# Performance work log

Measured on AMD Instinct MI355X. Metric: run time of the kernel, lower is better.

## Reference

```python
import jax, jax.numpy as jnp
import numpy as np

NUM_EXPERTS = 64
TOP_K = 2


def setup_inputs() -> dict:
    key = jax.random.key(0)
    k1, k2 = jax.random.split(key)
    B, D, E = 16384, 4096, NUM_EXPERTS
    routing_features = jax.random.normal(k1, (B, D), dtype=jnp.float32)
    # nn.Linear(D, E, bias=False) weight: [E, D], kaiming-uniform-ish init
    bound = 1.0 / np.sqrt(D)
    gate_w = jax.random.uniform(k2, (E, D), dtype=jnp.float32, minval=-bound, maxval=bound)
    return {"routing_features": routing_features, "gate_w": gate_w}


def reference(routing_features, gate_w):
    B = routing_features.shape[0]
    E, K = NUM_EXPERTS, TOP_K
    # linear gate (no bias): [B, E]
    logits = jnp.einsum("bd,ed->be", routing_features, gate_w)
    full_probs = jax.nn.softmax(logits, axis=-1)
    top_k_logits, top_k_indices = jax.lax.top_k(logits, K)  # [B, K]
    top_k_weights = jax.nn.softmax(top_k_logits, axis=-1)
    # load-balance loss: f_i = fraction of (token, slot) assignments to expert i
    tokens_per_expert = jnp.zeros((E,), dtype=jnp.float32).at[top_k_indices.reshape(-1)].add(1.0)
    f = tokens_per_expert / (B * K)
    P = full_probs.mean(axis=0)
    aux_loss = E * jnp.sum(f * P)
    return top_k_weights, top_k_indices, aux_loss
```

## Files before the change

kernel.cpp:

```cpp
#include <hip/hip_runtime.h>
#include <math.h>


typedef __attribute__((ext_vector_type(8))) short bf16x8;
typedef __attribute__((ext_vector_type(4))) float f32x4;

constexpr int B_ROWS  = 16384;
constexpr int D_DIM   = 4096;
constexpr int E_EXP   = 64;
constexpr int NTHR    = 512;
constexpr int TM      = 128;
constexpr int KSEG    = 256;
constexpr int NSPLIT  = D_DIM / KSEG;
constexpr int NS      = KSEG / 32;
constexpr int FLAGCAP = 8192;
constexpr float GAPTHR = 1e-3f;

__device__ __forceinline__ float wave_max64(float v) {
#pragma unroll
  for (int m = 32; m >= 1; m >>= 1) v = fmaxf(v, __shfl_xor(v, m, 64));
  return v;
}
__device__ __forceinline__ float wave_sum64(float v) {
#pragma unroll
  for (int m = 32; m >= 1; m >>= 1) v += __shfl_xor(v, m, 64);
  return v;
}
__device__ __forceinline__ void wave_argmax64(float v, int i, float& mv, int& mi) {
#pragma unroll
  for (int m = 32; m >= 1; m >>= 1) {
    float ov = __shfl_xor(v, m, 64);
    int   oi = __shfl_xor(i, m, 64);
    if (ov > v || (ov == v && oi < i)) { v = ov; i = oi; }
  }
  mv = v; mi = i;
}

__device__ __forceinline__ void async_copy16(void* lds_dst, const void* g_src) {
  auto g = (const __attribute__((address_space(1))) char*)(g_src);
  auto l = (__attribute__((address_space(3))) char*)(lds_dst);
  __builtin_amdgcn_global_load_lds(g, l, 16, 0, 0);
}

__device__ __forceinline__ void split8(const f32x4 a, const f32x4 b, bf16x8& hi, bf16x8& lo) {
  float f[8] = {a[0], a[1], a[2], a[3], b[0], b[1], b[2], b[3]};
#pragma unroll
  for (int i = 0; i < 8; ++i) {
    unsigned int u = __float_as_uint(f[i]);
    hi[i] = (short)(u >> 16);
    float rem = f[i] - __uint_as_float(u & 0xffff0000u);
    lo[i] = (short)(__float_as_uint(rem) >> 16);
  }
}

__global__ __launch_bounds__(NTHR) void wsplit(const float* __restrict__ gw,
                                               char* __restrict__ wsW,
                                               unsigned int* __restrict__ hdr) {
  const int n = blockIdx.x;
  const int t = threadIdx.x;
  if (n == 0 && t < 192) hdr[t] = 0u;
  const int lane = t & 63, h = (t >> 6) & 1, wc = t >> 7;
  const int col = wc * 16 + (lane & 15);
  const int k0  = n * 32 + (lane >> 4) * 8;
  const float* src = gw + (size_t)col * D_DIM + k0;
  union { unsigned short us[8]; uint4 v; } pk;
#pragma unroll
  for (int i = 0; i < 8; ++i) {
    float f = src[i];
    unsigned int u = __float_as_uint(f);
    if (h == 0) {
      pk.us[i] = (unsigned short)(u >> 16);
    } else {
      float rem = f - __uint_as_float(u & 0xffff0000u);
      pk.us[i] = (unsigned short)(__float_as_uint(rem) >> 16);
    }
  }
  *(uint4*)(wsW + (size_t)n * 8192 + (size_t)t * 16) = pk.v;
}

__global__ __launch_bounds__(NTHR) void gemm_partial(
    const float* __restrict__ rf, const char* __restrict__ wsW,
    float* __restrict__ part) {
  __shared__ char wlds[NS * 8192] __attribute__((aligned(16)));

  const int t = threadIdx.x, lane = t & 63, wv = t >> 6;
  const int ks   = blockIdx.x >> 7;
  const int rb   = blockIdx.x & 127;
  const int row0 = rb * TM;

  {
    const char* src = wsW + (size_t)ks * (NS * 8192);
#pragma unroll
    for (int i = 0; i < NS; ++i)
      async_copy16(wlds + i * 8192 + t * 16, src + i * 8192 + t * 16);
  }
  __syncthreads();

  const float* aptr = rf + (size_t)(row0 + wv * 16 + (lane & 15)) * D_DIM
                         + ks * KSEG + (lane >> 4) * 8;

  f32x4 acc[4] = {{0.f,0.f,0.f,0.f},{0.f,0.f,0.f,0.f},{0.f,0.f,0.f,0.f},{0.f,0.f,0.f,0.f}};
  f32x4 a0[4], a1[4];

#define LDA(s, n) { a0[s] = *(const f32x4*)(aptr + (n) * 32); \
                    a1[s] = *(const f32x4*)(aptr + (n) * 32 + 4); }

  LDA(0, 0); LDA(1, 1); LDA(2, 2); LDA(3, 3);
  __builtin_amdgcn_sched_barrier(0);

#pragma unroll
  for (int n = 0; n < NS; ++n) {
    const int s = n & 3;
    bf16x8 ahi, alo;
    split8(a0[s], a1[s], ahi, alo);
    if (n + 4 < NS) LDA(s, n + 4);
    __builtin_amdgcn_sched_barrier(0);
    const char* wn = wlds + n * 8192 + lane * 16;
#pragma unroll
    for (int cb = 0; cb < 4; ++cb) {
      bf16x8 whi = *(const bf16x8*)(wn + cb * 2048);
      bf16x8 wlo = *(const bf16x8*)(wn + cb * 2048 + 1024);
      acc[cb] = __builtin_amdgcn_mfma_f32_16x16x32_bf16(ahi, whi, acc[cb], 0, 0, 0);
      acc[cb] = __builtin_amdgcn_mfma_f32_16x16x32_bf16(alo, whi, acc[cb], 0, 0, 0);
      acc[cb] = __builtin_amdgcn_mfma_f32_16x16x32_bf16(ahi, wlo, acc[cb], 0, 0, 0);
    }
    __builtin_amdgcn_sched_barrier(0);
  }
#undef LDA

  const int colb = lane & 15;
  const int rowb = (lane >> 4) * 4;
  float* dst = part + ((size_t)ks * B_ROWS + row0 + wv * 16 + rowb) * E_EXP + colb;
#pragma unroll
  for (int cb = 0; cb < 4; ++cb)
#pragma unroll
    for (int j = 0; j < 4; ++j)
      dst[(size_t)j * E_EXP + cb * 16] = acc[cb][j];
}

__global__ __launch_bounds__(NTHR) void epilogue(
    const float* __restrict__ part, float* __restrict__ out,
    float* __restrict__ psum, unsigned int* __restrict__ cnt,
    int* __restrict__ flagcnt, int* __restrict__ flaglist) {
  __shared__ float pcol[E_EXP];
  __shared__ unsigned int scnt[E_EXP];

  const int t = threadIdx.x, lane = t & 63, wv = t >> 6;
  const int row0 = blockIdx.x * 64;

  if (t < E_EXP) { scnt[t] = 0; pcol[t] = 0.f; }
  __syncthreads();

#pragma unroll
  for (int j = 0; j < 8; ++j) {
    const int row = row0 + wv * 8 + j;
    float lg = 0.f;
#pragma unroll
    for (int s = 0; s < NSPLIT; ++s)
      lg += part[((size_t)s * B_ROWS + row) * E_EXP + lane];

    const float m  = wave_max64(lg);
    const float p  = __expf(lg - m);
    const float ss = wave_sum64(p);
    atomicAdd(&pcol[lane], p / ss);

    float v1; int i1; wave_argmax64(lg, lane, v1, i1);
    const float lm1 = (lane == i1) ? -INFINITY : lg;
    float v2; int i2; wave_argmax64(lm1, lane, v2, i2);
    const float lm2 = (lane == i2) ? -INFINITY : lm1;
    float v3; int i3; wave_argmax64(lm2, lane, v3, i3);
    if (lane == 0) {
      const float ex = expf(v2 - v1);
      out[row * 2 + 0] = 1.f / (1.f + ex);
      out[row * 2 + 1] = ex / (1.f + ex);
      out[2 * B_ROWS + row * 2 + 0] = (float)i1;
      out[2 * B_ROWS + row * 2 + 1] = (float)i2;
      atomicAdd(&scnt[i1], 1u);
      atomicAdd(&scnt[i2], 1u);
      if (v1 - v2 < GAPTHR || v2 - v3 < GAPTHR) {
        int fi = atomicAdd(flagcnt, 1);
        if (fi < FLAGCAP) flaglist[fi] = row;
      }
    }
  }
  __syncthreads();
  if (t < E_EXP) {
    atomicAdd(&psum[t], pcol[t]);
    const unsigned int c = scnt[t];
    if (c) atomicAdd(&cnt[t], c);
  }
}

__global__ __launch_bounds__(256) void cleanup(
    const float* __restrict__ rf, const float* __restrict__ gw,
    const int* __restrict__ flagcnt, const int* __restrict__ flaglist,
    const float* __restrict__ psum, const unsigned int* __restrict__ cnt,
    float* __restrict__ out) {
  __shared__ double sm[256];
  const int t = threadIdx.x;
  if (blockIdx.x == 0 && t < 64) {
    const float f = (float)cnt[t] / (float)(B_ROWS * 2);
    const float P = psum[t] / (float)B_ROWS;
    float v = wave_sum64(f * P);
    if (t == 0) out[4 * B_ROWS] = (float)E_EXP * v;
  }
  const int nf = min(*flagcnt, FLAGCAP);
  for (int fi = blockIdx.x; fi < nf; fi += gridDim.x) {
    const int row = flaglist[fi];
    const int e = t & 63, seg = t >> 6;
    const float* a = rf + (size_t)row * D_DIM + seg * 1024;
    const float* w = gw + (size_t)e * D_DIM + seg * 1024;
    double p0 = 0.0, p1 = 0.0, p2 = 0.0, p3 = 0.0;
    for (int k = 0; k < 1024; k += 4) {
      p0 = fma((double)a[k + 0], (double)w[k + 0], p0);
      p1 = fma((double)a[k + 1], (double)w[k + 1], p1);
      p2 = fma((double)a[k + 2], (double)w[k + 2], p2);
      p3 = fma((double)a[k + 3], (double)w[k + 3], p3);
    }
    sm[t] = (p0 + p1) + (p2 + p3);
    __syncthreads();
    if (t < 64) {
      const double l = sm[t] + sm[64 + t] + sm[128 + t] + sm[192 + t];
      double v = l; int ii = t;
#pragma unroll
      for (int m = 32; m >= 1; m >>= 1) {
        double ov = __shfl_xor(v, m, 64); int oi = __shfl_xor(ii, m, 64);
        if (ov > v || (ov == v && oi < ii)) { v = ov; ii = oi; }
      }
      const double v1 = v; const int i1 = ii;
      const double lm = (t == i1) ? -1e300 : l;
      v = lm; ii = t;
#pragma unroll
      for (int m = 32; m >= 1; m >>= 1) {
        double ov = __shfl_xor(v, m, 64); int oi = __shfl_xor(ii, m, 64);
        if (ov > v || (ov == v && oi < ii)) { v = ov; ii = oi; }
      }
      const double v2 = v; const int i2 = ii;
      if (t == 0) {
        const double ex = exp(v2 - v1);
        out[row * 2 + 0] = (float)(1.0 / (1.0 + ex));
        out[row * 2 + 1] = (float)(ex / (1.0 + ex));
        out[2 * B_ROWS + row * 2 + 0] = (float)i1;
        out[2 * B_ROWS + row * 2 + 1] = (float)i2;
      }
    }
    __syncthreads();
  }
}

extern "C" void kernel_launch(void* const* d_in, const int* in_sizes, int n_in,
                              void* d_out, int out_size, void* d_ws, size_t ws_size,
                              hipStream_t stream) {
  const float* rf = (const float*)d_in[0];
  const float* gw = (const float*)d_in[1];
  float* out = (float*)d_out;
  float* psum = (float*)d_ws;
  unsigned int* cnt = (unsigned int*)((char*)d_ws + 256);
  int* flagcnt = (int*)((char*)d_ws + 512);
  int* flaglist = (int*)((char*)d_ws + 768);
  char* wsW = (char*)d_ws + (1u << 20);
  float* part = (float*)((char*)d_ws + (2u << 20));

  wsplit<<<D_DIM / 32, NTHR, 0, stream>>>(gw, wsW, (unsigned int*)d_ws);
  gemm_partial<<<NSPLIT * (B_ROWS / TM), NTHR, 0, stream>>>(rf, wsW, part);
  epilogue<<<B_ROWS / 64, NTHR, 0, stream>>>(part, out, psum, cnt, flagcnt, flaglist);
  cleanup<<<64, 256, 0, stream>>>(rf, gw, flagcnt, flaglist, psum, cnt, out);
}
```

Measured before the change: 237.2 us.

## Fuse router GEMM with softmax/top-k epilogue using full-K row tiles

Replaces the split-K GEMM plus separate epilogue kernel with a single kernel in which each 256-thread block owns 16 rows across the full D dimension. Activation panels are staged through LDS with async copies, an XOR swizzle and double buffering, and the weight panels are streamed through a 4-deep ring with explicit vmcnt waits. Softmax, top-k, the flagging of near-ties and the aux-loss partial sums are then computed from LDS in the same kernel. This removes the partial-sum buffer write and reread, which for 16 K-splits is large, at the cost of each block re-reading the full weight matrix from L2 and having less parallelism per block.

```diff
diff --git a/kernel.cpp b/kernel.cpp
--- a/kernel.cpp
+++ b/kernel.cpp
@@ -9,10 +9,9 @@
 constexpr int D_DIM   = 4096;
 constexpr int E_EXP   = 64;
 constexpr int NTHR    = 512;
-constexpr int TM      = 128;
-constexpr int KSEG    = 256;
-constexpr int NSPLIT  = D_DIM / KSEG;
-constexpr int NS      = KSEG / 32;
+constexpr int GTHR    = 256;
+constexpr int TM      = 16;
+constexpr int NPAN    = 16;
 constexpr int FLAGCAP = 8192;
 constexpr float GAPTHR = 1e-3f;
 
@@ -78,92 +77,105 @@
   *(uint4*)(wsW + (size_t)n * 8192 + (size_t)t * 16) = pk.v;
 }
 
-__global__ __launch_bounds__(NTHR) void gemm_partial(
+__global__ __launch_bounds__(GTHR) void gemm_router(
     const float* __restrict__ rf, const char* __restrict__ wsW,
-    float* __restrict__ part) {
-  __shared__ char wlds[NS * 8192] __attribute__((aligned(16)));
+    float* __restrict__ out, float* __restrict__ psum,
+    unsigned int* __restrict__ cnt, int* __restrict__ flagcnt,
+    int* __restrict__ flaglist) {
+  __shared__ char lds[65536] __attribute__((aligned(16)));
+  __shared__ float pP[4][E_EXP];
+  __shared__ unsigned int scnt[E_EXP];
 
   const int t = threadIdx.x, lane = t & 63, wv = t >> 6;
-  const int ks   = blockIdx.x >> 7;
-  const int rb   = blockIdx.x & 127;
-  const int row0 = rb * TM;
-
-  {
-    const char* src = wsW + (size_t)ks * (NS * 8192);
-#pragma unroll
-    for (int i = 0; i < NS; ++i)
-      async_copy16(wlds + i * 8192 + t * 16, src + i * 8192 + t * 16);
-  }
+  const int row0 = blockIdx.x * TM;
+
+  int goffA[4];
+#pragma unroll
+  for (int j = 0; j < 4; ++j) {
+    const int q = j * GTHR + t;
+    const int row = q >> 6, ls = q & 63;
+    const int gs = (ls & ~7) | ((ls & 7) ^ (row & 7));
+    goffA[j] = (row0 + row) * D_DIM + gs * 4;
+  }
+
+  f32x4 acc = {0.f, 0.f, 0.f, 0.f};
+
+#define ISSUE_A(pan, sa)                                                      \
+  {                                                                           \
+    char* ad_ = lds + (sa) * 16384;                                           \
+    _Pragma("unroll") for (int j = 0; j < 4; ++j)                             \
+      async_copy16(ad_ + (j * GTHR + t) * 16, rf + goffA[j] + (pan) * 256);   \
+  }
+#define ISSUE_W(mm)                                                           \
+  {                                                                           \
+    char* wd_ = lds + 32768 + ((mm) & 3) * 8192;                              \
+    _Pragma("unroll") for (int j = 0; j < 2; ++j)                             \
+      async_copy16(wd_ + (j * GTHR + t) * 16,                                 \
+                   wsW + (size_t)(mm) * 8192 + (j * GTHR + t) * 16);          \
+  }
+
+#define PANEL(p, SA, LASTP)                                                   \
+  {                                                                           \
+    _Pragma("unroll")                                                         \
+    for (int s = 0; s < 8; ++s) {                                             \
+      if (LASTP) {                                                            \
+        if (s < 6)       asm volatile("s_waitcnt vmcnt(4)" ::: "memory");     \
+        else if (s == 6) asm volatile("s_waitcnt vmcnt(2)" ::: "memory");     \
+        else             asm volatile("s_waitcnt vmcnt(0)" ::: "memory");     \
+      } else {                                                                \
+        if (s == 1 || s == 2) asm volatile("s_waitcnt vmcnt(8)" ::: "memory");\
+        else                  asm volatile("s_waitcnt vmcnt(4)" ::: "memory");\
+      }                                                                       \
+      __builtin_amdgcn_s_barrier();                                           \
+      __builtin_amdgcn_sched_barrier(0);                                      \
+      const int m = (p) * 8 + s;                                              \
+      if (!(LASTP) && s == 0) ISSUE_A((p) + 1, (SA) ^ 1);                     \
+      if (!(LASTP) || s < 5) ISSUE_W(m + 3);                                  \
+      const char* ab = lds + (SA) * 16384 + (lane & 15) * 1024;               \
+      const int sl0 = s * 8 + (((lane >> 4) * 2 + 0) ^ (lane & 7));           \
+      const int sl1 = s * 8 + (((lane >> 4) * 2 + 1) ^ (lane & 7));           \
+      f32x4 fa = *(const f32x4*)(ab + sl0 * 16);                              \
+      f32x4 fb = *(const f32x4*)(ab + sl1 * 16);                              \
+      bf16x8 ahi, alo;                                                        \
+      split8(fa, fb, ahi, alo);                                               \
+      const char* wb = lds + 32768 + (m & 3) * 8192 + wv * 2048 + lane * 16;  \
+      const bf16x8 whi = *(const bf16x8*)(wb);                                \
+      const bf16x8 wlo = *(const bf16x8*)(wb + 1024);                         \
+      acc = __builtin_amdgcn_mfma_f32_16x16x32_bf16(ahi, whi, acc, 0, 0, 0);  \
+      acc = __builtin_amdgcn_mfma_f32_16x16x32_bf16(alo, whi, acc, 0, 0, 0);  \
+      acc = __builtin_amdgcn_mfma_f32_16x16x32_bf16(ahi, wlo, acc, 0, 0, 0);  \
+    }                                                                         \
+  }
+
+  ISSUE_A(0, 0);
+  ISSUE_W(0); ISSUE_W(1); ISSUE_W(2);
+
+  for (int p = 0; p < NPAN - 2; p += 2) {
+    PANEL(p, 0, false);
+    PANEL(p + 1, 1, false);
+  }
+  PANEL(NPAN - 2, 0, false);
+  PANEL(NPAN - 1, 1, true);
+#undef PANEL
+#undef ISSUE_A
+#undef ISSUE_W
+
+  float* lt = (float*)lds;
+  if (t < E_EXP) scnt[t] = 0;
+#pragma unroll
+  for (int j = 0; j < 4; ++j)
+    lt[((lane >> 4) * 4 + j) * 65 + wv * 16 + (lane & 15)] = acc[j];
   __syncthreads();
 
-  const float* aptr = rf + (size_t)(row0 + wv * 16 + (lane & 15)) * D_DIM
-                         + ks * KSEG + (lane >> 4) * 8;
-
-  f32x4 acc[4] = {{0.f,0.f,0.f,0.f},{0.f,0.f,0.f,0.f},{0.f,0.f,0.f,0.f},{0.f,0.f,0.f,0.f}};
-  f32x4 a0[4], a1[4];
-
-#define LDA(s, n) { a0[s] = *(const f32x4*)(aptr + (n) * 32); \
-                    a1[s] = *(const f32x4*)(aptr + (n) * 32 + 4); }
-
-  LDA(0, 0); LDA(1, 1); LDA(2, 2); LDA(3, 3);
-  __builtin_amdgcn_sched_barrier(0);
-
-#pragma unroll
-  for (int n = 0; n < NS; ++n) {
-    const int s = n & 3;
-    bf16x8 ahi, alo;
-    split8(a0[s], a1[s], ahi, alo);
-    if (n + 4 < NS) LDA(s, n + 4);
-    __builtin_amdgcn_sched_barrier(0);
-    const char* wn = wlds + n * 8192 + lane * 16;
-#pragma unroll
-    for (int cb = 0; cb < 4; ++cb) {
-      bf16x8 whi = *(const bf16x8*)(wn + cb * 2048);
-      bf16x8 wlo = *(const bf16x8*)(wn + cb * 2048 + 1024);
-      acc[cb] = __builtin_amdgcn_mfma_f32_16x16x32_bf16(ahi, whi, acc[cb], 0, 0, 0);
-      acc[cb] = __builtin_amdgcn_mfma_f32_16x16x32_bf16(alo, whi, acc[cb], 0, 0, 0);
-      acc[cb] = __builtin_amdgcn_mfma_f32_16x16x32_bf16(ahi, wlo, acc[cb], 0, 0, 0);
-    }
-    __builtin_amdgcn_sched_barrier(0);
-  }
-#undef LDA
-
-  const int colb = lane & 15;
-  const int rowb = (lane >> 4) * 4;
-  float* dst = part + ((size_t)ks * B_ROWS + row0 + wv * 16 + rowb) * E_EXP + colb;
-#pragma unroll
-  for (int cb = 0; cb < 4; ++cb)
-#pragma unroll
-    for (int j = 0; j < 4; ++j)
-      dst[(size_t)j * E_EXP + cb * 16] = acc[cb][j];
-}
-
-__global__ __launch_bounds__(NTHR) void epilogue(
-    const float* __restrict__ part, float* __restrict__ out,
-    float* __restrict__ psum, unsigned int* __restrict__ cnt,
-    int* __restrict__ flagcnt, int* __restrict__ flaglist) {
-  __shared__ float pcol[E_EXP];
-  __shared__ unsigned int scnt[E_EXP];
-
-  const int t = threadIdx.x, lane = t & 63, wv = t >> 6;
-  const int row0 = blockIdx.x * 64;
-
-  if (t < E_EXP) { scnt[t] = 0; pcol[t] = 0.f; }
-  __syncthreads();
-
-#pragma unroll
-  for (int j = 0; j < 8; ++j) {
-    const int row = row0 + wv * 8 + j;
-    float lg = 0.f;
-#pragma unroll
-    for (int s = 0; s < NSPLIT; ++s)
-      lg += part[((size_t)s * B_ROWS + row) * E_EXP + lane];
-
-    const float m  = wave_max64(lg);
-    const float p  = __expf(lg - m);
-    const float ss = wave_sum64(p);
-    atomicAdd(&pcol[lane], p / ss);
-
+  float Pacc = 0.f;
+#pragma unroll
+  for (int jr = 0; jr < 4; ++jr) {
+    const int r = wv * 4 + jr;
+    const float lg = lt[r * 65 + lane];
+    const float mx = wave_max64(lg);
+    const float pe = __expf(lg - mx);
+    const float ss = wave_sum64(pe);
+    Pacc += pe / ss;
     float v1; int i1; wave_argmax64(lg, lane, v1, i1);
     const float lm1 = (lane == i1) ? -INFINITY : lg;
     float v2; int i2; wave_argmax64(lm1, lane, v2, i2);
@@ -171,6 +183,7 @@
     float v3; int i3; wave_argmax64(lm2, lane, v3, i3);
     if (lane == 0) {
       const float ex = expf(v2 - v1);
+      const int row = row0 + r;
       out[row * 2 + 0] = 1.f / (1.f + ex);
       out[row * 2 + 1] = ex / (1.f + ex);
       out[2 * B_ROWS + row * 2 + 0] = (float)i1;
@@ -183,9 +196,10 @@
       }
     }
   }
+  pP[wv][lane] = Pacc;
   __syncthreads();
   if (t < E_EXP) {
-    atomicAdd(&psum[t], pcol[t]);
+    atomicAdd(&psum[t], pP[0][t] + pP[1][t] + pP[2][t] + pP[3][t]);
     const unsigned int c = scnt[t];
     if (c) atomicAdd(&cnt[t], c);
   }
@@ -259,10 +273,9 @@
   int* flagcnt = (int*)((char*)d_ws + 512);
   int* flaglist = (int*)((char*)d_ws + 768);
   char* wsW = (char*)d_ws + (1u << 20);
-  float* part = (float*)((char*)d_ws + (2u << 20));
 
   wsplit<<<D_DIM / 32, NTHR, 0, stream>>>(gw, wsW, (unsigned int*)d_ws);
-  gemm_partial<<<NSPLIT * (B_ROWS / TM), NTHR, 0, stream>>>(rf, wsW, part);
-  epilogue<<<B_ROWS / 64, NTHR, 0, stream>>>(part, out, psum, cnt, flagcnt, flaglist);
+  gemm_router<<<B_ROWS / TM, GTHR, 0, stream>>>(rf, wsW, out, psum, cnt,
+                                                flagcnt, flaglist);
   cleanup<<<64, 256, 0, stream>>>(rf, gw, flagcnt, flaglist, psum, cnt, out);
 }
```

Result: slower. 257.5 us (+8.6%).
